# Kernel tuning notes

Measured on AMD Instinct MI355X. Metric: run time of the kernel, lower is better.

## Reference

```python
import jax, jax.numpy as jnp
import numpy as np
import math

B, S, H, NH = 8, 2048, 128, 4
DH = H // NH
SQRT_2_OVER_PI = math.sqrt(2.0 / math.pi)


def layer_norm(x, a, b, eps=1e-6):
    # Faithful to the torch module: unbiased std (ddof=1) and divide by (std + eps)
    mean = jnp.mean(x, axis=-1, keepdims=True)
    std = jnp.std(x, axis=-1, keepdims=True, ddof=1)
    return a * (x - mean) / (std + eps) + b


def setup_inputs() -> dict:
    key = jax.random.key(0)
    ks = jax.random.split(key, 10)
    inp = {
        "hidden": jax.random.normal(ks[0], (B, S, H), dtype=jnp.float32),
        "mask": jax.random.randint(ks[1], (B, S), 0, 2, dtype=jnp.int32),
        # attention params
        "attn_scale_w": jax.random.normal(ks[2], (NH, S), dtype=jnp.float32) * 0.1,
        "Wl": jax.random.normal(ks[3], (H, H), dtype=jnp.float32) * (1.0 / math.sqrt(H)),
        "bl": jnp.zeros((H,), dtype=jnp.float32),
        # FFN params
        "W1": jax.random.normal(ks[4], (H, H), dtype=jnp.float32) * (1.0 / math.sqrt(H)),
        "b1": jnp.zeros((H,), dtype=jnp.float32),
        "ffn_scale_w": jax.random.normal(ks[5], (S, 1), dtype=jnp.float32) * 0.1,
        # layer norms
        "ln1_a": jnp.ones((H,), dtype=jnp.float32),
        "ln1_b": jnp.zeros((H,), dtype=jnp.float32),
        "ln2_a": jnp.ones((H,), dtype=jnp.float32),
        "ln2_b": jnp.zeros((H,), dtype=jnp.float32),
    }
    return inp


def reference(hidden, mask, attn_scale_w, Wl, bl, W1, b1, ffn_scale_w,
              ln1_a, ln1_b, ln2_a, ln2_b):
    x = hidden  # [B, S, H]

    # --- attention sublayer (pre-norm residual) ---
    n1 = layer_norm(x, ln1_a, ln1_b)
    qkv = n1.reshape(B, S, NH, DH).transpose(0, 2, 1, 3)  # [B, NH, S, DH]
    # scores with per-head/per-query-position learned scale
    corr = jnp.einsum("bhqd,bhkd->bhqk", qkv, qkv) / math.sqrt(DH)
    corr = corr * attn_scale_w[None, :, :, None]  # scale over query positions
    # mask over key positions: [B,1,1,S], broadcast matches repeat in torch
    corr = jnp.where(mask[:, None, None, :] == 0, -1e9, corr)
    prob = jax.nn.softmax(corr, axis=-1)
    h = jnp.einsum("bhqk,bhkd->bhqd", prob, qkv)
    h = h.transpose(0, 2, 1, 3).reshape(B, S, H)
    attn_out = h @ Wl.T + bl
    x = x + attn_out

    # --- FFN sublayer (pre-norm residual) ---
    n2 = layer_norm(x, ln2_a, ln2_b)
    hf = ffn_scale_w[None] * (n2 @ W1.T + b1)  # [B, S, H] with per-position scale
    act = 0.5 * hf * (1.0 + jnp.tanh(SQRT_2_OVER_PI * (hf + 0.044715 * hf ** 3)))
    x = x + act

    return x
```

## Files before the change

kernel.cpp:

```cpp
#include <hip/hip_runtime.h>

#define BB 8
#define SS 2048
#define HH 128
#define NHH 4
#define DHH 32

typedef _Float16 f16;
typedef f16 f16x4 __attribute__((ext_vector_type(4)));
typedef f16 f16x8 __attribute__((ext_vector_type(8)));
typedef float f32x4 __attribute__((ext_vector_type(4)));

__device__ __forceinline__ f16x8 cat(f16x4 a, f16x4 b) {
  return (f16x8){a[0], a[1], a[2], a[3], b[0], b[1], b[2], b[3]};
}

__device__ __forceinline__ f16x4 tr_read(const f16* p) {
  f16x4 d;
  asm volatile("ds_read_b64_tr_b16 %0, %1"
               : "=v"(d)
               : "v"((__attribute__((address_space(3))) const f16*)p)
               : "memory");
  return d;
}

__global__ __launch_bounds__(256) void stage1_kernel(const float* __restrict__ x,
                                                     const float* __restrict__ ga,
                                                     const float* __restrict__ gb,
                                                     const float* __restrict__ Wl,
                                                     const float* __restrict__ W1,
                                                     const int* __restrict__ mask,
                                                     f16* __restrict__ n1,
                                                     f16* __restrict__ Wlf,
                                                     f16* __restrict__ W1f,
                                                     int* __restrict__ idx,
                                                     int* __restrict__ nkcnt,
                                                     int* __restrict__ nkpad) {
  const int tid = threadIdx.x;
  if (blockIdx.x < 1024) {
    const int wave = tid >> 6, lane = tid & 63;
    const int grp = lane >> 4, lm = lane & 15;
    const int r = wave * 4 + grp;
    const size_t row = (size_t)blockIdx.x * 16 + r;

    const float* xr = x + row * HH + lm * 8;
    float4 v0 = *(const float4*)(xr);
    float4 v1 = *(const float4*)(xr + 4);
    float xv[8] = {v0.x, v0.y, v0.z, v0.w, v1.x, v1.y, v1.z, v1.w};
    float sum = 0.f, sq = 0.f;
#pragma unroll
    for (int j = 0; j < 8; ++j) { sum += xv[j]; sq += xv[j] * xv[j]; }
#pragma unroll
    for (int m = 1; m < 16; m <<= 1) {
      sum += __shfl_xor(sum, m);
      sq += __shfl_xor(sq, m);
    }
    float mean = sum * (1.0f / HH);
    float var = fmaxf((sq - (float)HH * mean * mean) * (1.0f / (HH - 1)), 0.0f);
    float inv = 1.0f / (sqrtf(var) + 1e-6f);

    float4 a0 = *(const float4*)(ga + lm * 8);
    float4 a1 = *(const float4*)(ga + lm * 8 + 4);
    float4 b0 = *(const float4*)(gb + lm * 8);
    float4 b1 = *(const float4*)(gb + lm * 8 + 4);
    float av[8] = {a0.x, a0.y, a0.z, a0.w, a1.x, a1.y, a1.z, a1.w};
    float bv[8] = {b0.x, b0.y, b0.z, b0.w, b1.x, b1.y, b1.z, b1.w};
    f16x8 w;
#pragma unroll
    for (int j = 0; j < 8; ++j) w[j] = (f16)(av[j] * (xv[j] - mean) * inv + bv[j]);
    *(f16x8*)(n1 + row * HH + lm * 8) = w;
    return;
  }
  if (blockIdx.x < 1056) {
    int g = (blockIdx.x - 1024) * 256 + tid;
    if (g < 4096) {
      float4 w = ((const float4*)Wl)[g];
      f16x4 o = {(f16)w.x, (f16)w.y, (f16)w.z, (f16)w.w};
      ((f16x4*)Wlf)[g] = o;
    } else {
      float4 w = ((const float4*)W1)[g - 4096];
      f16x4 o = {(f16)w.x, (f16)w.y, (f16)w.z, (f16)w.w};
      ((f16x4*)W1f)[g - 4096] = o;
    }
    return;
  }
  const int b = blockIdx.x - 1056;
  __shared__ int ps[256];
  int m8[8];
  int cnt = 0;
  const int* mp = mask + b * SS + tid * 8;
#pragma unroll
  for (int j = 0; j < 8; ++j) {
    m8[j] = mp[j];
    cnt += (m8[j] != 0);
  }
  ps[tid] = cnt;
  __syncthreads();
  for (int off = 1; off < 256; off <<= 1) {
    int v = (tid >= off) ? ps[tid - off] : 0;
    __syncthreads();
    ps[tid] += v;
    __syncthreads();
  }
  int pos = ps[tid] - cnt;
#pragma unroll
  for (int j = 0; j < 8; ++j) {
    if (m8[j] != 0) idx[b * SS + pos++] = tid * 8 + j;
  }
  __syncthreads();
  int nkv = ps[255];
  int npv = (nkv + 63) & ~63;
  if (npv == 0) npv = 64;
  for (int jj = nkv + tid; jj < npv; jj += 256) idx[b * SS + jj] = 0;
  if (tid == 255) { nkcnt[b] = nkv; nkpad[b] = npv; }
}

__global__ __launch_bounds__(256, 2) void attn_kernel(const f16* __restrict__ n1,
                                                      const int* __restrict__ idx,
                                                      const int* __restrict__ nkcnt,
                                                      const int* __restrict__ nkpad,
                                                      const float* __restrict__ scalew,
                                                      f16* __restrict__ hatt) {
  const int tid = threadIdx.x;
  const int qb = blockIdx.x & 15;
  const int h = (blockIdx.x >> 4) & 3;
  const int b = blockIdx.x >> 6;
  const int wave = tid >> 6, lane = tid & 63;
  const int lg = lane >> 4, lm = lane & 15;
  const int nk = nkcnt[b];
  const int ns = nkpad[b] >> 6;

  __shared__ __align__(16) f16 Kt[4][2][2][64][16];
  __shared__ __align__(16) int idxL[SS];

  const f16* __restrict__ nb = n1 + (size_t)b * SS * HH + h * DHH;
  f16* __restrict__ tile = &Kt[wave][0][0][0][0];

  for (int j = tid * 4; j < (ns << 6); j += 1024)
    *(int4*)&idxL[j] = *(const int4*)(idx + b * SS + j);

  const int q0 = qb * 128 + wave * 32 + lm;
  f16x8 qf[2];
#pragma unroll
  for (int qt = 0; qt < 2; ++qt) {
    int q = q0 + qt * 16;
    f16x8 raw = *(const f16x8*)(nb + (size_t)q * HH + lg * 8);
    f16 s = (f16)(scalew[h * SS + q] * 0.2550680718664f);
#pragma unroll
    for (int j = 0; j < 8; ++j) raw[j] *= s;
    qf[qt] = raw;
  }

  const int sk = lane >> 2, sp = lane & 3;

  const f32x4 zero = {0.f, 0.f, 0.f, 0.f};
  f32x4 acc[2][2] = {{zero, zero}, {zero, zero}};
  f32x4 lacc[2] = {zero, zero};
  const f16x8 ones = {(f16)1, (f16)1, (f16)1, (f16)1, (f16)1, (f16)1, (f16)1, (f16)1};

  __syncthreads();

#pragma unroll
  for (int i = 0; i < 4; ++i) {
    int row = idxL[i * 16 + sk];
    f16x8 v = *(const f16x8*)(nb + (size_t)row * HH + sp * 8);
    *(f16x8*)(tile + (sp >> 1) * 1024 + (i * 16 + sk) * 16 + (sp & 1) * 8) = v;
  }

  for (int c = 0; c < ns; ++c) {
    const int bo = (c & 1) * 2048;
    const int k0 = c * 64;
    f16x8 kreg[4];
    const bool more = (c + 1 < ns);
    if (more) {
#pragma unroll
      for (int i = 0; i < 4; ++i) {
        int row = idxL[k0 + 64 + i * 16 + sk];
        kreg[i] = *(const f16x8*)(nb + (size_t)row * HH + sp * 8);
      }
    }

    f16x4 t0a = tr_read(tile + bo + 0 + lane * 4);
    f16x4 t0b = tr_read(tile + bo + 256 + lane * 4);
    f16x4 t0c = tr_read(tile + bo + 512 + lane * 4);
    f16x4 t0d = tr_read(tile + bo + 768 + lane * 4);
    f16x4 t1a = tr_read(tile + bo + 1024 + lane * 4);
    f16x4 t1b = tr_read(tile + bo + 1280 + lane * 4);
    f16x4 t1c = tr_read(tile + bo + 1536 + lane * 4);
    f16x4 t1d = tr_read(tile + bo + 1792 + lane * 4);

    f16x8 kf[4];
#pragma unroll
    for (int t = 0; t < 4; ++t)
      kf[t] = *(const f16x8*)(tile + bo + (lg >> 1) * 1024 + (t * 16 + lm) * 16 + (lg & 1) * 8);

    const bool tail = (k0 + 64 > nk);
    f16x8 pf[2][2];
#define PF_LOOP(MASKED)                                                                   \
  _Pragma("unroll") for (int qt = 0; qt < 2; ++qt) {                                      \
    _Pragma("unroll") for (int t = 0; t < 4; ++t) {                                       \
      f32x4 st = __builtin_amdgcn_mfma_f32_16x16x32_f16(kf[t], qf[qt], zero, 0, 0, 0);    \
      _Pragma("unroll") for (int r = 0; r < 4; ++r) {                                     \
        float pe = __builtin_amdgcn_exp2f(st[r]);                                         \
        if (MASKED && (k0 + t * 16 + lg * 4 + r >= nk)) pe = 0.0f;                        \
        pf[qt][t >> 1][(t & 1) * 4 + r] = (f16)pe;                                        \
      }                                                                                   \
    }                                                                                     \
  }
    if (!tail) { PF_LOOP(false) } else { PF_LOOP(true) }
#undef PF_LOOP

#pragma unroll
    for (int qt = 0; qt < 2; ++qt) {
#pragma unroll
      for (int s = 0; s < 2; ++s)
        lacc[qt] = __builtin_amdgcn_mfma_f32_16x16x32_f16(ones, pf[qt][s], lacc[qt], 0, 0, 0);
    }

    asm volatile("s_waitcnt lgkmcnt(0)" ::: "memory");
    __builtin_amdgcn_sched_barrier(0);

    f16x8 vf;
    vf = cat(t0a, t0b);
#pragma unroll
    for (int qt = 0; qt < 2; ++qt)
      acc[qt][0] = __builtin_amdgcn_mfma_f32_16x16x32_f16(vf, pf[qt][0], acc[qt][0], 0, 0, 0);
    vf = cat(t1a, t1b);
#pragma unroll
    for (int qt = 0; qt < 2; ++qt)
      acc[qt][1] = __builtin_amdgcn_mfma_f32_16x16x32_f16(vf, pf[qt][0], acc[qt][1], 0, 0, 0);
    vf = cat(t0c, t0d);
#pragma unroll
    for (int qt = 0; qt < 2; ++qt)
      acc[qt][0] = __builtin_amdgcn_mfma_f32_16x16x32_f16(vf, pf[qt][1], acc[qt][0], 0, 0, 0);
    vf = cat(t1c, t1d);
#pragma unroll
    for (int qt = 0; qt < 2; ++qt)
      acc[qt][1] = __builtin_amdgcn_mfma_f32_16x16x32_f16(vf, pf[qt][1], acc[qt][1], 0, 0, 0);

    if (more) {
      const int bn = 2048 - (c & 1) * 2048;
#pragma unroll
      for (int i = 0; i < 4; ++i)
        *(f16x8*)(tile + bn + (sp >> 1) * 1024 + (i * 16 + sk) * 16 + (sp & 1) * 8) = kreg[i];
    }
  }

#pragma unroll
  for (int qt = 0; qt < 2; ++qt) {
    float inv = 1.0f / lacc[qt][0];
    int q = q0 + qt * 16;
    f16* op = hatt + (size_t)(b * SS + q) * HH + h * DHH;
    f16x4 o0 = {(f16)(acc[qt][0][0] * inv), (f16)(acc[qt][0][1] * inv),
                (f16)(acc[qt][0][2] * inv), (f16)(acc[qt][0][3] * inv)};
    f16x4 o1 = {(f16)(acc[qt][1][0] * inv), (f16)(acc[qt][1][1] * inv),
                (f16)(acc[qt][1][2] * inv), (f16)(acc[qt][1][3] * inv)};
    *(f16x4*)(op + lg * 4) = o0;
    *(f16x4*)(op + 16 + lg * 4) = o1;
  }
}

__global__ __launch_bounds__(256) void mlp_kernel(const f16* __restrict__ X,
                                                  const f16* __restrict__ Wlf,
                                                  const float* __restrict__ bl,
                                                  const float* __restrict__ resid,
                                                  const float* __restrict__ ln2a,
                                                  const float* __restrict__ ln2b,
                                                  const f16* __restrict__ W1f,
                                                  const float* __restrict__ b1,
                                                  const float* __restrict__ fscale,
                                                  float* __restrict__ out) {
  const int tid = threadIdx.x;
  const int wave = tid >> 6, lane = tid & 63;
  const int lg = lane >> 4, lm = lane & 15;
  const int rbase = blockIdx.x * 32;
  const int nc0 = wave * 32;

  __shared__ __align__(16) f16 n2t[32][136];
  __shared__ float red[4][32][2];

  f32x4 acc[2][2] = {};
  const f16* xr0 = X + (size_t)(rbase + lm) * HH;
  const f16* xr1 = X + (size_t)(rbase + 16 + lm) * HH;
#pragma unroll
  for (int ks = 0; ks < 4; ++ks) {
    f16x8 bf0 = *(const f16x8*)(xr0 + ks * 32 + lg * 8);
    f16x8 bf1 = *(const f16x8*)(xr1 + ks * 32 + lg * 8);
#pragma unroll
    for (int nt = 0; nt < 2; ++nt) {
      f16x8 af = *(const f16x8*)(Wlf + (size_t)(nc0 + nt * 16 + lm) * HH + ks * 32 + lg * 8);
      acc[0][nt] = __builtin_amdgcn_mfma_f32_16x16x32_f16(af, bf0, acc[0][nt], 0, 0, 0);
      acc[1][nt] = __builtin_amdgcn_mfma_f32_16x16x32_f16(af, bf1, acc[1][nt], 0, 0, 0);
    }
  }
  float sum[2] = {0.f, 0.f}, sq[2] = {0.f, 0.f};
  f32x4 o[2][2];
#pragma unroll
  for (int g = 0; g < 2; ++g) {
    int row = rbase + g * 16 + lm;
#pragma unroll
    for (int nt = 0; nt < 2; ++nt) {
      int n = nc0 + nt * 16 + lg * 4;
      float4 rv = *(const float4*)(resid + (size_t)row * HH + n);
      float4 bv = *(const float4*)(bl + n);
      f32x4 v = acc[g][nt];
      v[0] += rv.x + bv.x; v[1] += rv.y + bv.y;
      v[2] += rv.z + bv.z; v[3] += rv.w + bv.w;
      o[g][nt] = v;
      sum[g] += v[0] + v[1] + v[2] + v[3];
      sq[g] += v[0] * v[0] + v[1] * v[1] + v[2] * v[2] + v[3] * v[3];
    }
    sum[g] += __shfl_xor(sum[g], 16); sum[g] += __shfl_xor(sum[g], 32);
    sq[g] += __shfl_xor(sq[g], 16);  sq[g] += __shfl_xor(sq[g], 32);
  }
  if (lane < 16) {
#pragma unroll
    for (int g = 0; g < 2; ++g) {
      red[wave][g * 16 + lm][0] = sum[g];
      red[wave][g * 16 + lm][1] = sq[g];
    }
  }
  __syncthreads();
#pragma unroll
  for (int g = 0; g < 2; ++g) {
    int lr = g * 16 + lm;
    float ts = red[0][lr][0] + red[1][lr][0] + red[2][lr][0] + red[3][lr][0];
    float tq = red[0][lr][1] + red[1][lr][1] + red[2][lr][1] + red[3][lr][1];
    float mean = ts * (1.0f / HH);
    float var = fmaxf((tq - (float)HH * mean * mean) * (1.0f / (HH - 1)), 0.0f);
    float inv = 1.0f / (sqrtf(var) + 1e-6f);
#pragma unroll
    for (int nt = 0; nt < 2; ++nt) {
      int n = nc0 + nt * 16 + lg * 4;
      float4 av = *(const float4*)(ln2a + n);
      float4 b2 = *(const float4*)(ln2b + n);
      f16x4 w;
      w[0] = (f16)(av.x * (o[g][nt][0] - mean) * inv + b2.x);
      w[1] = (f16)(av.y * (o[g][nt][1] - mean) * inv + b2.y);
      w[2] = (f16)(av.z * (o[g][nt][2] - mean) * inv + b2.z);
      w[3] = (f16)(av.w * (o[g][nt][3] - mean) * inv + b2.w);
      *(f16x4*)(&n2t[lr][n]) = w;
    }
  }
  __syncthreads();

  f32x4 fa[2][2] = {};
#pragma unroll
  for (int ks = 0; ks < 4; ++ks) {
    f16x8 bf0 = *(const f16x8*)(&n2t[lm][ks * 32 + lg * 8]);
    f16x8 bf1 = *(const f16x8*)(&n2t[16 + lm][ks * 32 + lg * 8]);
#pragma unroll
    for (int nt = 0; nt < 2; ++nt) {
      f16x8 af = *(const f16x8*)(W1f + (size_t)(nc0 + nt * 16 + lm) * HH + ks * 32 + lg * 8);
      fa[0][nt] = __builtin_amdgcn_mfma_f32_16x16x32_f16(af, bf0, fa[0][nt], 0, 0, 0);
      fa[1][nt] = __builtin_amdgcn_mfma_f32_16x16x32_f16(af, bf1, fa[1][nt], 0, 0, 0);
    }
  }
#pragma unroll
  for (int g = 0; g < 2; ++g) {
    int row = rbase + g * 16 + lm;
    float fs = fscale[row & (SS - 1)];
#pragma unroll
    for (int nt = 0; nt < 2; ++nt) {
      int n = nc0 + nt * 16 + lg * 4;
      float4 bv = *(const float4*)(b1 + n);
      const float* bp = &bv.x;
#pragma unroll
      for (int e = 0; e < 4; ++e) {
        float hf = fs * (fa[g][nt][e] + bp[e]);
        float u = 0.7978845608028654f * hf * (1.0f + 0.044715f * hf * hf);
        float ex = __builtin_amdgcn_exp2f(u * 2.8853900817779268f);
        float t = 1.0f - 2.0f / (ex + 1.0f);
        o[g][nt][e] += 0.5f * hf * (1.0f + t);
      }
      *(f32x4*)(out + (size_t)row * HH + n) = o[g][nt];
    }
  }
}

extern "C" void kernel_launch(void* const* d_in, const int* in_sizes, int n_in,
                              void* d_out, int out_size, void* d_ws, size_t ws_size,
                              hipStream_t stream) {
  const float* hidden = (const float*)d_in[0];
  const int* mask = (const int*)d_in[1];
  const float* scalew = (const float*)d_in[2];
  const float* Wl = (const float*)d_in[3];
  const float* bl = (const float*)d_in[4];
  const float* W1 = (const float*)d_in[5];
  const float* b1 = (const float*)d_in[6];
  const float* fscale = (const float*)d_in[7];
  const float* ln1a = (const float*)d_in[8];
  const float* ln1b = (const float*)d_in[9];
  const float* ln2a = (const float*)d_in[10];
  const float* ln2b = (const float*)d_in[11];
  float* out = (float*)d_out;

  const size_t NE = (size_t)BB * SS * HH;
  f16* n1 = (f16*)d_ws;
  f16* hattf = n1 + NE;
  f16* Wlf = hattf + NE;
  f16* W1f = Wlf + HH * HH;
  int* idx = (int*)(W1f + HH * HH);
  int* nkcnt = idx + BB * SS;
  int* nkpad = nkcnt + BB;

  stage1_kernel<<<1064, 256, 0, stream>>>(hidden, ln1a, ln1b, Wl, W1, mask,
                                          n1, Wlf, W1f, idx, nkcnt, nkpad);
  attn_kernel<<<BB * NHH * (SS / 128), 256, 0, stream>>>(n1, idx, nkcnt, nkpad,
                                                         scalew, hattf);
  mlp_kernel<<<BB * SS / 32, 256, 0, stream>>>(hattf, Wlf, bl, hidden, ln2a, ln2b,
                                               W1f, b1, fscale, out);
}
```

Baseline: 40.75 us.

## Process two key chunks per attention iteration with deeper prefetch

Unrolls the attention key loop so each iteration handles two 64-key chunks from two per-wave LDS tiles. It issues global loads for the next two chunks before computing, and writes them back to LDS afterwards. The aim is to keep more memory traffic in flight and amortise the LDS wait and scheduling barrier over twice the MFMA work. In exchange, register pressure rises (two sets of staged K rows, transposed reads and K fragments), which may hurt occupancy under launch_bounds(256,2).

```diff
diff --git a/kernel.cpp b/kernel.cpp
--- a/kernel.cpp
+++ b/kernel.cpp
@@ -130,11 +130,12 @@
   const int nk = nkcnt[b];
   const int ns = nkpad[b] >> 6;
 
-  __shared__ __align__(16) f16 Kt[4][2][2][64][16];
+  __shared__ __align__(16) f16 Kt[4][2][2048];
   __shared__ __align__(16) int idxL[SS];
 
   const f16* __restrict__ nb = n1 + (size_t)b * SS * HH + h * DHH;
-  f16* __restrict__ tile = &Kt[wave][0][0][0][0];
+  f16* __restrict__ tA = &Kt[wave][0][0];
+  f16* __restrict__ tB = &Kt[wave][1][0];
 
   for (int j = tid * 4; j < (ns << 6); j += 1024)
     *(int4*)&idxL[j] = *(const int4*)(idx + b * SS + j);
@@ -158,93 +159,103 @@
   f32x4 lacc[2] = {zero, zero};
   const f16x8 ones = {(f16)1, (f16)1, (f16)1, (f16)1, (f16)1, (f16)1, (f16)1, (f16)1};
 
+#define STAGE_LOAD(KR, C)                                                                \
+  _Pragma("unroll") for (int i = 0; i < 4; ++i) {                                        \
+    int row_ = idxL[(C) * 64 + i * 16 + sk];                                             \
+    KR[i] = *(const f16x8*)(nb + (size_t)row_ * HH + sp * 8);                            \
+  }
+#define STAGE_WRITE(TILE, KR)                                                            \
+  _Pragma("unroll") for (int i = 0; i < 4; ++i)                                          \
+    *(f16x8*)((TILE) + (sp >> 1) * 1024 + (i * 16 + sk) * 16 + (sp & 1) * 8) = KR[i];
+
+#define CHUNK_COMPUTE(TR, KF, K0)                                                        \
+  {                                                                                      \
+    const int k0_ = (K0);                                                                \
+    const bool tail_ = (k0_ + 64 > nk);                                                  \
+    f16x8 pf[2][2];                                                                      \
+    if (!tail_) {                                                                        \
+      _Pragma("unroll") for (int qt = 0; qt < 2; ++qt)                                   \
+        _Pragma("unroll") for (int t = 0; t < 4; ++t) {                                  \
+          f32x4 st = __builtin_amdgcn_mfma_f32_16x16x32_f16(KF[t], qf[qt], zero, 0, 0, 0);\
+          _Pragma("unroll") for (int r = 0; r < 4; ++r)                                  \
+            pf[qt][t >> 1][(t & 1) * 4 + r] = (f16)__builtin_amdgcn_exp2f(st[r]);        \
+        }                                                                                \
+    } else {                                                                             \
+      _Pragma("unroll") for (int qt = 0; qt < 2; ++qt)                                   \
+        _Pragma("unroll") for (int t = 0; t < 4; ++t) {                                  \
+          f32x4 st = __builtin_amdgcn_mfma_f32_16x16x32_f16(KF[t], qf[qt], zero, 0, 0, 0);\
+          _Pragma("unroll") for (int r = 0; r < 4; ++r) {                                \
+            float pe = __builtin_amdgcn_exp2f(st[r]);                                    \
+            if (k0_ + t * 16 + lg * 4 + r >= nk) pe = 0.0f;                              \
+            pf[qt][t >> 1][(t & 1) * 4 + r] = (f16)pe;                                   \
+          }                                                                              \
+        }                                                                                \
+    }                                                                                    \
+    _Pragma("unroll") for (int qt = 0; qt < 2; ++qt)                                     \
+      _Pragma("unroll") for (int s = 0; s < 2; ++s)                                      \
+        lacc[qt] = __builtin_amdgcn_mfma_f32_16x16x32_f16(ones, pf[qt][s], lacc[qt], 0, 0, 0);\
+    f16x8 vf;                                                                            \
+    vf = cat(TR[0], TR[1]);                                                              \
+    _Pragma("unroll") for (int qt = 0; qt < 2; ++qt)                                     \
+      acc[qt][0] = __builtin_amdgcn_mfma_f32_16x16x32_f16(vf, pf[qt][0], acc[qt][0], 0, 0, 0);\
+    vf = cat(TR[4], TR[5]);                                                              \
+    _Pragma("unroll") for (int qt = 0; qt < 2; ++qt)                                     \
+      acc[qt][1] = __builtin_amdgcn_mfma_f32_16x16x32_f16(vf, pf[qt][0], acc[qt][1], 0, 0, 0);\
+    vf = cat(TR[2], TR[3]);                                                              \
+    _Pragma("unroll") for (int qt = 0; qt < 2; ++qt)                                     \
+      acc[qt][0] = __builtin_amdgcn_mfma_f32_16x16x32_f16(vf, pf[qt][1], acc[qt][0], 0, 0, 0);\
+    vf = cat(TR[6], TR[7]);                                                              \
+    _Pragma("unroll") for (int qt = 0; qt < 2; ++qt)                                     \
+      acc[qt][1] = __builtin_amdgcn_mfma_f32_16x16x32_f16(vf, pf[qt][1], acc[qt][1], 0, 0, 0);\
+  }
+
   __syncthreads();
 
-#pragma unroll
-  for (int i = 0; i < 4; ++i) {
-    int row = idxL[i * 16 + sk];
-    f16x8 v = *(const f16x8*)(nb + (size_t)row * HH + sp * 8);
-    *(f16x8*)(tile + (sp >> 1) * 1024 + (i * 16 + sk) * 16 + (sp & 1) * 8) = v;
-  }
-
-  for (int c = 0; c < ns; ++c) {
-    const int bo = (c & 1) * 2048;
-    const int k0 = c * 64;
-    f16x8 kreg[4];
-    const bool more = (c + 1 < ns);
-    if (more) {
-#pragma unroll
-      for (int i = 0; i < 4; ++i) {
-        int row = idxL[k0 + 64 + i * 16 + sk];
-        kreg[i] = *(const f16x8*)(nb + (size_t)row * HH + sp * 8);
-      }
-    }
-
-    f16x4 t0a = tr_read(tile + bo + 0 + lane * 4);
-    f16x4 t0b = tr_read(tile + bo + 256 + lane * 4);
-    f16x4 t0c = tr_read(tile + bo + 512 + lane * 4);
-    f16x4 t0d = tr_read(tile + bo + 768 + lane * 4);
-    f16x4 t1a = tr_read(tile + bo + 1024 + lane * 4);
-    f16x4 t1b = tr_read(tile + bo + 1280 + lane * 4);
-    f16x4 t1c = tr_read(tile + bo + 1536 + lane * 4);
-    f16x4 t1d = tr_read(tile + bo + 1792 + lane * 4);
-
-    f16x8 kf[4];
+  {
+    f16x8 kr[4];
+    STAGE_LOAD(kr, 0)
+    STAGE_WRITE(tA, kr)
+    if (ns > 1) {
+      STAGE_LOAD(kr, 1)
+      STAGE_WRITE(tB, kr)
+    }
+  }
+
+  for (int cc = 0; cc < ns; cc += 2) {
+    const bool hasB = (cc + 1 < ns);
+    const bool pA = (cc + 2 < ns), pB = (cc + 3 < ns);
+    f16x8 krA[4], krB[4];
+    if (pA) STAGE_LOAD(krA, cc + 2)
+    if (pB) STAGE_LOAD(krB, cc + 3)
+
+    f16x4 trA[8];
+    f16x8 kfA[4];
+#pragma unroll
+    for (int u = 0; u < 8; ++u) trA[u] = tr_read(tA + u * 256 + lane * 4);
 #pragma unroll
     for (int t = 0; t < 4; ++t)
-      kf[t] = *(const f16x8*)(tile + bo + (lg >> 1) * 1024 + (t * 16 + lm) * 16 + (lg & 1) * 8);
-
-    const bool tail = (k0 + 64 > nk);
-    f16x8 pf[2][2];
-#define PF_LOOP(MASKED)                                                                   \
-  _Pragma("unroll") for (int qt = 0; qt < 2; ++qt) {                                      \
-    _Pragma("unroll") for (int t = 0; t < 4; ++t) {                                       \
-      f32x4 st = __builtin_amdgcn_mfma_f32_16x16x32_f16(kf[t], qf[qt], zero, 0, 0, 0);    \
-      _Pragma("unroll") for (int r = 0; r < 4; ++r) {                                     \
-        float pe = __builtin_amdgcn_exp2f(st[r]);                                         \
-        if (MASKED && (k0 + t * 16 + lg * 4 + r >= nk)) pe = 0.0f;                        \
-        pf[qt][t >> 1][(t & 1) * 4 + r] = (f16)pe;                                        \
-      }                                                                                   \
-    }                                                                                     \
-  }
-    if (!tail) { PF_LOOP(false) } else { PF_LOOP(true) }
-#undef PF_LOOP
-
-#pragma unroll
-    for (int qt = 0; qt < 2; ++qt) {
-#pragma unroll
-      for (int s = 0; s < 2; ++s)
-        lacc[qt] = __builtin_amdgcn_mfma_f32_16x16x32_f16(ones, pf[qt][s], lacc[qt], 0, 0, 0);
-    }
-
+      kfA[t] = *(const f16x8*)(tA + (lg >> 1) * 1024 + (t * 16 + lm) * 16 + (lg & 1) * 8);
+    f16x4 trB[8];
+    f16x8 kfB[4];
+    if (hasB) {
+#pragma unroll
+      for (int u = 0; u < 8; ++u) trB[u] = tr_read(tB + u * 256 + lane * 4);
+#pragma unroll
+      for (int t = 0; t < 4; ++t)
+        kfB[t] = *(const f16x8*)(tB + (lg >> 1) * 1024 + (t * 16 + lm) * 16 + (lg & 1) * 8);
+    }
     asm volatile("s_waitcnt lgkmcnt(0)" ::: "memory");
     __builtin_amdgcn_sched_barrier(0);
 
-    f16x8 vf;
-    vf = cat(t0a, t0b);
-#pragma unroll
-    for (int qt = 0; qt < 2; ++qt)
-      acc[qt][0] = __builtin_amdgcn_mfma_f32_16x16x32_f16(vf, pf[qt][0], acc[qt][0], 0, 0, 0);
-    vf = cat(t1a, t1b);
-#pragma unroll
-    for (int qt = 0; qt < 2; ++qt)
-      acc[qt][1] = __builtin_amdgcn_mfma_f32_16x16x32_f16(vf, pf[qt][0], acc[qt][1], 0, 0, 0);
-    vf = cat(t0c, t0d);
-#pragma unroll
-    for (int qt = 0; qt < 2; ++qt)
-      acc[qt][0] = __builtin_amdgcn_mfma_f32_16x16x32_f16(vf, pf[qt][1], acc[qt][0], 0, 0, 0);
-    vf = cat(t1c, t1d);
-#pragma unroll
-    for (int qt = 0; qt < 2; ++qt)
-      acc[qt][1] = __builtin_amdgcn_mfma_f32_16x16x32_f16(vf, pf[qt][1], acc[qt][1], 0, 0, 0);
-
-    if (more) {
-      const int bn = 2048 - (c & 1) * 2048;
-#pragma unroll
-      for (int i = 0; i < 4; ++i)
-        *(f16x8*)(tile + bn + (sp >> 1) * 1024 + (i * 16 + sk) * 16 + (sp & 1) * 8) = kreg[i];
-    }
-  }
+    CHUNK_COMPUTE(trA, kfA, cc * 64)
+    if (hasB) CHUNK_COMPUTE(trB, kfB, (cc + 1) * 64)
+
+    if (pA) STAGE_WRITE(tA, krA)
+    if (pB) STAGE_WRITE(tB, krB)
+  }
+#undef STAGE_LOAD
+#undef STAGE_WRITE
+#undef CHUNK_COMPUTE
 
 #pragma unroll
   for (int qt = 0; qt < 2; ++qt) {
```

Result: slower. 41.80 us (+2.6%).
